# Optimization experiments

Hardware: AMD Instinct MI355X
Metric: run time of the kernel (lower is better)

Reference implementation:

```python
import jax, jax.numpy as jnp
import numpy as np

NEG_BIG = -9e15
ALPHA = 0.2  # leakyrelu slope

N, IN_F, OUT_F = 8192, 512, 64


def setup_inputs() -> dict:
    key = jax.random.key(0)
    ks = jax.random.split(key, 7)
    return {
        "input": jax.random.normal(ks[0], (N, IN_F), dtype=jnp.float32),
        "W": jax.random.normal(ks[1], (IN_F, OUT_F), dtype=jnp.float32) * 0.05,
        "a": jax.random.normal(ks[2], (2 * OUT_F, 1), dtype=jnp.float32) * 0.1,
        "W_si": jax.random.normal(ks[3], (1, 1), dtype=jnp.float32),
        "W_ei": jax.random.normal(ks[4], (1, 1), dtype=jnp.float32),
        "adj_ad": jax.random.uniform(ks[5], (N, N), dtype=jnp.float32),
        "adj": jax.random.randint(ks[6], (N, N), 0, 2, dtype=jnp.int32),
    }


def reference(input, W, a, W_si, W_ei, adj_ad, adj):
    h = input @ W                                   # [N, F]
    F_ = h.shape[1]
    a1, a2 = a[:F_, 0], a[F_:, 0]                   # split concat projection
    # concat-score: a^T [h_i || h_j] == (h@a1)_i + (h@a2)_j, no [N,N,2F] tensor
    e = jax.nn.leaky_relu(h @ a1[:, None] + (h @ a2[:, None]).T, ALPHA)  # [N, N]
    e = jnp.abs(W_ei) * e + jnp.abs(W_si) * adj_ad
    attention = jnp.where(adj > 0, e, jnp.float32(NEG_BIG))
    attention = jax.nn.softmax(attention, axis=1)
    # dropout is identity in eval mode (training=False)
    h_prime = attention @ h                         # [N, F]
    return jax.nn.elu(h_prime)
```

## Files before the change

### kernel.cpp

```cpp
#include <hip/hip_runtime.h>
#include <math.h>

#define N 8192
#define IN_F 512
#define OUTF 64
#define TI 16

typedef _Float16 f16x8 __attribute__((ext_vector_type(8)));
typedef float f32x4 __attribute__((ext_vector_type(4)));

#define OFF_HT   0u
#define OFF_S    262144u
#define OFF_T    270336u
#define OFF_TMAX 278528u

__device__ __forceinline__ unsigned enc_f32(float f) {
  unsigned b = __float_as_uint(f);
  return b ^ ((unsigned)((int)b >> 31) | 0x80000000u);
}

__global__ __launch_bounds__(64) void k_precompute(
    const float* __restrict__ input, const float* __restrict__ W,
    const float* __restrict__ a, _Float16* __restrict__ hT,
    float* __restrict__ s, float* __restrict__ t) {
  const int lane = threadIdx.x;
  const int i0 = blockIdx.x * 4;

  float acc[4] = {0.f, 0.f, 0.f, 0.f};
  for (int c = 0; c < IN_F; c += 4) {
    const float w0 = W[(c + 0) * OUTF + lane];
    const float w1 = W[(c + 1) * OUTF + lane];
    const float w2 = W[(c + 2) * OUTF + lane];
    const float w3 = W[(c + 3) * OUTF + lane];
    #pragma unroll
    for (int r = 0; r < 4; r++) {
      const float4 iv = *(const float4*)(input + (size_t)(i0 + r) * IN_F + c);
      acc[r] += iv.x * w0 + iv.y * w1 + iv.z * w2 + iv.w * w3;
    }
  }

  union { _Float16 f[4]; uint2 u; } pk;
  #pragma unroll
  for (int r = 0; r < 4; r++) pk.f[r] = (_Float16)acc[r];
  *(uint2*)(hT + (size_t)lane * N + i0) = pk.u;

  const float a1v = a[lane];
  const float a2v = a[OUTF + lane];
  #pragma unroll
  for (int r = 0; r < 4; r++) {
    float sv = acc[r] * a1v;
    float tv = acc[r] * a2v;
    #pragma unroll
    for (int off = 1; off < 64; off <<= 1) {
      sv += __shfl_xor(sv, off);
      tv += __shfl_xor(tv, off);
    }
    if (lane == 0) {
      s[i0 + r] = sv;
      t[i0 + r] = tv;
    }
  }
}

__global__ __launch_bounds__(512) void k_tmax(const float* __restrict__ t,
                                              unsigned* __restrict__ tmax) {
  __shared__ float red[8];
  const int tid = threadIdx.x;
  float m = t[blockIdx.x * 512 + tid];
  #pragma unroll
  for (int off = 1; off < 64; off <<= 1) m = fmaxf(m, __shfl_xor(m, off));
  if ((tid & 63) == 0) red[tid >> 6] = m;
  __syncthreads();
  if (tid == 0) {
    #pragma unroll
    for (int w = 1; w < 8; w++) m = fmaxf(m, red[w]);
    atomicMax(tmax, enc_f32(m));
  }
}

__global__ __launch_bounds__(256, 4) void k_attn(
    const _Float16* __restrict__ hT, const float* __restrict__ s,
    const float* __restrict__ t, const unsigned* __restrict__ tmaxp,
    const float* __restrict__ W_si, const float* __restrict__ W_ei,
    const float* __restrict__ adj_ad, const int* __restrict__ adj,
    float* __restrict__ out) {
  __shared__ float aLDS[4 * 1024];
  __shared__ float sLDS[4 * 64];

  const int tid = threadIdx.x;
  const int wave = tid >> 6;
  const int lane = tid & 63;
  const int q = lane >> 4;
  const int m = lane & 15;
  const int i0 = blockIdx.x * TI;
  const int off = blockIdx.x & 15;

  const float aei = fabsf(W_ei[0]);
  const float asi = fabsf(W_si[0]);
  const unsigned te = *tmaxp;
  const float tm = __uint_as_float((te & 0x80000000u) ? (te ^ 0x80000000u) : ~te);

  const float sr = s[i0 + m];
  const float xm = sr + tm;
  const float Mr = aei * fmaxf(xm, 0.2f * xm) + asi;

  float S = 0.f;
  f32x4 acc[4];
  #pragma unroll
  for (int nb = 0; nb < 4; nb++) acc[nb] = (f32x4){0.f, 0.f, 0.f, 0.f};

  const size_t rowA = (size_t)(i0 + m) * N;

  auto CB = [&](int c) -> int {
    return ((((((c >> 2) + off) & 15) << 4) + (wave << 2) + (c & 3)) << 5) +
           (q << 3);
  };

  struct Pf { float4 a0, a1, t0, t1; int4 k0, k1; };

  auto LOADC = [&](int c) -> Pf {
    const int cb = CB(c);
    Pf p;
    p.a0 = *(const float4*)(adj_ad + rowA + cb);
    p.a1 = *(const float4*)(adj_ad + rowA + cb + 4);
    p.k0 = *(const int4*)(adj + rowA + cb);
    p.k1 = *(const int4*)(adj + rowA + cb + 4);
    p.t0 = *(const float4*)(t + cb);
    p.t1 = *(const float4*)(t + cb + 4);
    return p;
  };

  auto LHT = [&](int c, f16x8* fb) {
    const int cb = CB(c);
    #pragma unroll
    for (int nb = 0; nb < 4; nb++)
      fb[nb] = *(const f16x8*)(hT + (size_t)(nb * 16 + m) * N + cb);
  };

  auto COMPUTE = [&](const Pf& p, const f16x8* fb) {
    const float ad[8] = {p.a0.x, p.a0.y, p.a0.z, p.a0.w,
                         p.a1.x, p.a1.y, p.a1.z, p.a1.w};
    const int mk[8] = {p.k0.x, p.k0.y, p.k0.z, p.k0.w,
                       p.k1.x, p.k1.y, p.k1.z, p.k1.w};
    const float tv[8] = {p.t0.x, p.t0.y, p.t0.z, p.t0.w,
                         p.t1.x, p.t1.y, p.t1.z, p.t1.w};
    f16x8 fa;
    #pragma unroll
    for (int e = 0; e < 8; e++) {
      const float x = sr + tv[e];
      const float ee = aei * fmaxf(x, 0.2f * x) + asi * ad[e];
      const float pv = (mk[e] > 0) ? __expf(ee - Mr) : 0.f;
      S += pv;
      fa[e] = (_Float16)pv;
    }
    #pragma unroll
    for (int nb = 0; nb < 4; nb++)
      acc[nb] = __builtin_amdgcn_mfma_f32_16x16x32_f16(fa, fb[nb], acc[nb],
                                                       0, 0, 0);
  };

  Pf pa = LOADC(0);
  #pragma unroll 1
  for (int c = 0; c < 64; c += 2) {
    f16x8 fbA[4];
    LHT(c, fbA);
    Pf pb = LOADC(c + 1);
    COMPUTE(pa, fbA);
    f16x8 fbB[4];
    LHT(c + 1, fbB);
    pa = LOADC((c + 2) & 63);
    COMPUTE(pb, fbB);
  }

  sLDS[wave * 64 + lane] = S;
  #pragma unroll
  for (int nb = 0; nb < 4; nb++) {
    #pragma unroll
    for (int reg = 0; reg < 4; reg++) {
      aLDS[wave * 1024 + (q * 4 + reg) * 64 + nb * 16 + m] = acc[nb][reg];
    }
  }
  __syncthreads();

  #pragma unroll
  for (int ii = 0; ii < 4; ii++) {
    const int e = tid + 256 * ii;
    const int r = e >> 6;
    const int f = e & 63;
    float num = 0.f, den = 0.f;
    #pragma unroll
    for (int w = 0; w < 4; w++) {
      num += aLDS[w * 1024 + r * 64 + f];
      #pragma unroll
      for (int qq = 0; qq < 4; qq++) den += sLDS[w * 64 + qq * 16 + r];
    }
    const float x = num / den;
    out[(size_t)(i0 + r) * OUTF + f] = x > 0.f ? x : expm1f(x);
  }
}

extern "C" void kernel_launch(void* const* d_in, const int* in_sizes, int n_in,
                              void* d_out, int out_size, void* d_ws, size_t ws_size,
                              hipStream_t stream) {
  const float* input  = (const float*)d_in[0];
  const float* W      = (const float*)d_in[1];
  const float* a      = (const float*)d_in[2];
  const float* W_si   = (const float*)d_in[3];
  const float* W_ei   = (const float*)d_in[4];
  const float* adj_ad = (const float*)d_in[5];
  const int*   adj    = (const int*)d_in[6];
  float* out = (float*)d_out;
  float* ws  = (float*)d_ws;

  _Float16* hT   = (_Float16*)(ws + OFF_HT);
  float* s       = ws + OFF_S;
  float* t       = ws + OFF_T;
  unsigned* tmax = (unsigned*)(ws + OFF_TMAX);

  hipMemsetAsync(tmax, 0, 4, stream);
  k_precompute<<<N / 4, 64, 0, stream>>>(input, W, a, hT, s, t);
  k_tmax<<<N / 512, 512, 0, stream>>>(t, tmax);
  k_attn<<<N / TI, 256, 0, stream>>>(hT, s, t, tmax, W_si, W_ei,
                                     adj_ad, adj, out);
}
```

Before: 705.7 us.

## Restructure attention kernel to stage exp weights in LDS with software pipeline

The attention kernel now uses 512 threads, and each half-wave handles one query row over contiguous 256-column tiles. Each lane computes its exp weights and writes them as fp16 into a double-buffered LDS tile. The MFMA for the previous tile runs from that LDS tile while the next adj/adj_ad tile loads, with explicit sched barriers and a wave barrier per tile. |W_ei| is folded into s and t in the precompute kernel, and the mask is applied by multiplying instead of a select. The aim is coalesced row-contiguous streaming of the large N×N inputs and overlap of loads with compute, at the cost of LDS traffic and a block barrier every tile.

Measured after the change: 578.4 us. 18.0% less time.

```diff
diff --git a/kernel.cpp b/kernel.cpp
--- a/kernel.cpp
+++ b/kernel.cpp
@@ -5,6 +5,9 @@
 #define IN_F 512
 #define OUTF 64
 #define TI 16
+#define JT 256
+#define NTILE (N / JT)
+#define PS 264
 
 typedef _Float16 f16x8 __attribute__((ext_vector_type(8)));
 typedef float f32x4 __attribute__((ext_vector_type(4)));
@@ -14,6 +17,14 @@
 #define OFF_T    270336u
 #define OFF_TMAX 278528u
 
+#define SB0() __builtin_amdgcn_sched_barrier(0)
+#define SYNC()                                           \
+  SB0();                                                 \
+  asm volatile("s_waitcnt lgkmcnt(0)" ::: "memory");     \
+  SB0();                                                 \
+  __builtin_amdgcn_s_barrier();                          \
+  SB0();
+
 __device__ __forceinline__ unsigned enc_f32(float f) {
   unsigned b = __float_as_uint(f);
   return b ^ ((unsigned)((int)b >> 31) | 0x80000000u);
@@ -21,10 +32,12 @@
 
 __global__ __launch_bounds__(64) void k_precompute(
     const float* __restrict__ input, const float* __restrict__ W,
-    const float* __restrict__ a, _Float16* __restrict__ hT,
-    float* __restrict__ s, float* __restrict__ t) {
+    const float* __restrict__ a, const float* __restrict__ W_ei,
+    _Float16* __restrict__ hT, float* __restrict__ s2,
+    float* __restrict__ t2) {
   const int lane = threadIdx.x;
   const int i0 = blockIdx.x * 4;
+  const float aei = fabsf(W_ei[0]);
 
   float acc[4] = {0.f, 0.f, 0.f, 0.f};
   for (int c = 0; c < IN_F; c += 4) {
@@ -56,8 +69,8 @@
       tv += __shfl_xor(tv, off);
     }
     if (lane == 0) {
-      s[i0 + r] = sv;
-      t[i0 + r] = tv;
+      s2[i0 + r] = aei * sv;
+      t2[i0 + r] = aei * tv;
     }
   }
 }
@@ -78,122 +91,153 @@
   }
 }
 
-__global__ __launch_bounds__(256, 4) void k_attn(
-    const _Float16* __restrict__ hT, const float* __restrict__ s,
-    const float* __restrict__ t, const unsigned* __restrict__ tmaxp,
+__global__ __launch_bounds__(512, 4) void k_attn(
+    const _Float16* __restrict__ hT, const float* __restrict__ s2,
+    const float* __restrict__ t2, const unsigned* __restrict__ tmaxp,
     const float* __restrict__ W_si, const float* __restrict__ W_ei,
     const float* __restrict__ adj_ad, const int* __restrict__ adj,
     float* __restrict__ out) {
-  __shared__ float aLDS[4 * 1024];
-  __shared__ float sLDS[4 * 64];
+  __shared__ __align__(16) float smem[8224];
+  _Float16* P = (_Float16*)smem;
 
   const int tid = threadIdx.x;
-  const int wave = tid >> 6;
+  const int w = tid >> 6;
   const int lane = tid & 63;
   const int q = lane >> 4;
   const int m = lane & 15;
+  const int h2 = lane >> 5;
+  const int cw = lane & 31;
   const int i0 = blockIdx.x * TI;
-  const int off = blockIdx.x & 15;
-
-  const float aei = fabsf(W_ei[0]);
+
   const float asi = fabsf(W_si[0]);
+  (void)W_ei;
   const unsigned te = *tmaxp;
-  const float tm = __uint_as_float((te & 0x80000000u) ? (te ^ 0x80000000u) : ~te);
-
-  const float sr = s[i0 + m];
-  const float xm = sr + tm;
-  const float Mr = aei * fmaxf(xm, 0.2f * xm) + asi;
+  const float tm2 = __uint_as_float((te & 0x80000000u) ? (te ^ 0x80000000u) : ~te);
+
+  const int myrow = 2 * w + h2;
+  const float s2r = s2[i0 + myrow];
+  const float ym = s2r + tm2;
+  const float MrB = fmaxf(ym, 0.2f * ym) + asi;
 
   float S = 0.f;
   f32x4 acc[4];
   #pragma unroll
   for (int nb = 0; nb < 4; nb++) acc[nb] = (f32x4){0.f, 0.f, 0.f, 0.f};
 
-  const size_t rowA = (size_t)(i0 + m) * N;
-
-  auto CB = [&](int c) -> int {
-    return ((((((c >> 2) + off) & 15) << 4) + (wave << 2) + (c & 3)) << 5) +
-           (q << 3);
-  };
-
-  struct Pf { float4 a0, a1, t0, t1; int4 k0, k1; };
-
-  auto LOADC = [&](int c) -> Pf {
-    const int cb = CB(c);
-    Pf p;
-    p.a0 = *(const float4*)(adj_ad + rowA + cb);
-    p.a1 = *(const float4*)(adj_ad + rowA + cb + 4);
-    p.k0 = *(const int4*)(adj + rowA + cb);
-    p.k1 = *(const int4*)(adj + rowA + cb + 4);
-    p.t0 = *(const float4*)(t + cb);
-    p.t1 = *(const float4*)(t + cb + 4);
+  const size_t gRow = (size_t)(i0 + myrow) * N;
+  const int c0 = cw * 4;
+
+  struct PF { float4 a0, a1; int4 k0, k1; };
+
+  auto LOADT = [&](int kt) -> PF {
+    const size_t b = gRow + (size_t)kt * JT + c0;
+    PF p;
+    p.a0 = *(const float4*)(adj_ad + b);
+    p.a1 = *(const float4*)(adj_ad + b + 128);
+    p.k0 = *(const int4*)(adj + b);
+    p.k1 = *(const int4*)(adj + b + 128);
     return p;
   };
 
-  auto LHT = [&](int c, f16x8* fb) {
-    const int cb = CB(c);
-    #pragma unroll
-    for (int nb = 0; nb < 4; nb++)
-      fb[nb] = *(const f16x8*)(hT + (size_t)(nb * 16 + m) * N + cb);
-  };
-
-  auto COMPUTE = [&](const Pf& p, const f16x8* fb) {
+  auto EXPW = [&](int kt, const PF& p, const float4& tva, const float4& tvb) {
     const float ad[8] = {p.a0.x, p.a0.y, p.a0.z, p.a0.w,
                          p.a1.x, p.a1.y, p.a1.z, p.a1.w};
     const int mk[8] = {p.k0.x, p.k0.y, p.k0.z, p.k0.w,
                        p.k1.x, p.k1.y, p.k1.z, p.k1.w};
-    const float tv[8] = {p.t0.x, p.t0.y, p.t0.z, p.t0.w,
-                         p.t1.x, p.t1.y, p.t1.z, p.t1.w};
-    f16x8 fa;
+    const float tv[8] = {tva.x, tva.y, tva.z, tva.w,
+                         tvb.x, tvb.y, tvb.z, tvb.w};
+    union { _Float16 hh[8]; uint2 u[2]; } pk;
     #pragma unroll
     for (int e = 0; e < 8; e++) {
-      const float x = sr + tv[e];
-      const float ee = aei * fmaxf(x, 0.2f * x) + asi * ad[e];
-      const float pv = (mk[e] > 0) ? __expf(ee - Mr) : 0.f;
+      const float y = s2r + tv[e];
+      const float lr = fmaxf(y, 0.2f * y);
+      const float arg = fmaf(asi, ad[e], lr - MrB);
+      const float pv = __expf(arg) * (float)mk[e];
       S += pv;
-      fa[e] = (_Float16)pv;
-    }
-    #pragma unroll
-    for (int nb = 0; nb < 4; nb++)
-      acc[nb] = __builtin_amdgcn_mfma_f32_16x16x32_f16(fa, fb[nb], acc[nb],
-                                                       0, 0, 0);
+      pk.hh[e] = (_Float16)pv;
+    }
+    _Float16* dst = P + (kt & 1) * (16 * PS) + myrow * PS;
+    *(uint2*)(dst + c0) = pk.u[0];
+    *(uint2*)(dst + c0 + 128) = pk.u[1];
   };
 
-  Pf pa = LOADC(0);
+  #define MLOAD(kt, FB, FA)                                                   \
+    {                                                                         \
+      const int cb_ = (kt) * JT + w * 32 + q * 8;                             \
+      _Pragma("unroll") for (int nb = 0; nb < 4; nb++)                        \
+          FB[nb] = *(const f16x8*)(hT + (size_t)(nb * 16 + m) * N + cb_);     \
+      FA = *(const f16x8*)(P + ((kt) & 1) * (16 * PS) + m * PS + w * 32 +     \
+                           q * 8);                                            \
+    }
+
+  #define MSTEP(FB, FA)                                                       \
+    {                                                                         \
+      _Pragma("unroll") for (int nb = 0; nb < 4; nb++)                        \
+          acc[nb] = __builtin_amdgcn_mfma_f32_16x16x32_f16(FA, FB[nb],        \
+                                                           acc[nb], 0, 0, 0);\
+    }
+
+  PF pA = LOADT(0);
+  PF pB;
+
   #pragma unroll 1
-  for (int c = 0; c < 64; c += 2) {
-    f16x8 fbA[4];
-    LHT(c, fbA);
-    Pf pb = LOADC(c + 1);
-    COMPUTE(pa, fbA);
-    f16x8 fbB[4];
-    LHT(c + 1, fbB);
-    pa = LOADC((c + 2) & 63);
-    COMPUTE(pb, fbB);
-  }
-
-  sLDS[wave * 64 + lane] = S;
+  for (int k = 0; k < NTILE; k += 2) {
+    {
+      const float4 tva = *(const float4*)(t2 + k * JT + c0);
+      const float4 tvb = *(const float4*)(t2 + k * JT + c0 + 128);
+      f16x8 fb[4], fa;
+      if (k >= 1) MLOAD(k - 1, fb, fa);
+      SB0();
+      pB = LOADT(k + 1);
+      SB0();
+      if (k >= 1) MSTEP(fb, fa);
+      EXPW(k, pA, tva, tvb);
+      SYNC();
+    }
+    {
+      const float4 tva = *(const float4*)(t2 + (k + 1) * JT + c0);
+      const float4 tvb = *(const float4*)(t2 + (k + 1) * JT + c0 + 128);
+      f16x8 fb[4], fa;
+      MLOAD(k, fb, fa);
+      SB0();
+      if (k + 2 < NTILE) pA = LOADT(k + 2);
+      SB0();
+      MSTEP(fb, fa);
+      EXPW(k + 1, pB, tva, tvb);
+      SYNC();
+    }
+  }
+
+  {
+    f16x8 fb[4], fa;
+    MLOAD(NTILE - 1, fb, fa);
+    MSTEP(fb, fa);
+  }
+
+  #pragma unroll
+  for (int off = 1; off < 32; off <<= 1) S += __shfl_xor(S, off);
+
+  SYNC();
+
+  if ((lane & 31) == 0) smem[8192 + myrow] = S;
   #pragma unroll
   for (int nb = 0; nb < 4; nb++) {
     #pragma unroll
     for (int reg = 0; reg < 4; reg++) {
-      aLDS[wave * 1024 + (q * 4 + reg) * 64 + nb * 16 + m] = acc[nb][reg];
+      smem[w * 1024 + (q * 4 + reg) * 64 + nb * 16 + m] = acc[nb][reg];
     }
   }
   __syncthreads();
 
   #pragma unroll
-  for (int ii = 0; ii < 4; ii++) {
-    const int e = tid + 256 * ii;
+  for (int ii = 0; ii < 2; ii++) {
+    const int e = tid + 512 * ii;
     const int r = e >> 6;
     const int f = e & 63;
-    float num = 0.f, den = 0.f;
-    #pragma unroll
-    for (int w = 0; w < 4; w++) {
-      num += aLDS[w * 1024 + r * 64 + f];
-      #pragma unroll
-      for (int qq = 0; qq < 4; qq++) den += sLDS[w * 64 + qq * 16 + r];
-    }
+    float num = 0.f;
+    #pragma unroll
+    for (int ww = 0; ww < 8; ww++) num += smem[ww * 1024 + r * 64 + f];
+    const float den = smem[8192 + r];
     const float x = num / den;
     out[(size_t)(i0 + r) * OUTF + f] = x > 0.f ? x : expm1f(x);
   }
@@ -213,13 +257,13 @@
   float* ws  = (float*)d_ws;
 
   _Float16* hT   = (_Float16*)(ws + OFF_HT);
-  float* s       = ws + OFF_S;
-  float* t       = ws + OFF_T;
+  float* s2      = ws + OFF_S;
+  float* t2      = ws + OFF_T;
   unsigned* tmax = (unsigned*)(ws + OFF_TMAX);
 
   hipMemsetAsync(tmax, 0, 4, stream);
-  k_precompute<<<N / 4, 64, 0, stream>>>(input, W, a, hT, s, t);
-  k_tmax<<<N / 512, 512, 0, stream>>>(t, tmax);
-  k_attn<<<N / TI, 256, 0, stream>>>(hT, s, t, tmax, W_si, W_ei,
+  k_precompute<<<N / 4, 64, 0, stream>>>(input, W, a, W_ei, hT, s2, t2);
+  k_tmax<<<N / 512, 512, 0, stream>>>(t2, tmax);
+  k_attn<<<N / TI, 512, 0, stream>>>(hT, s2, t2, tmax, W_si, W_ei,
                                      adj_ad, adj, out);
 }
```
